# Kernel tuning notes

Hardware: AMD Instinct MI355X
Metric: run time of the kernel (lower is better)

## Reference

```python
import jax, jax.numpy as jnp
import numpy as np

B, N, DE, DH, L, DC = 8, 256, 768, 192, 2, 192
NEG = 1e30  # mask_logic constant from the repo


def setup_inputs() -> dict:
    ks = iter(jax.random.split(jax.random.key(0), 32))

    def nrm(shape, s=0.02):
        return jax.random.normal(next(ks), shape, dtype=jnp.float32) * s

    features = jax.random.normal(next(ks), (B, N, DE), dtype=jnp.float32)
    # DAG adjacency: node i attends to a subset of j < i; guarantee edge (i, i-1)
    rnd = jax.random.bernoulli(next(ks), 0.3, (B, N, N))
    tril = jnp.tril(jnp.ones((N, N), jnp.bool_), -1)
    adj = ((rnd & tril[None]) | jnp.eye(N, k=-1, dtype=jnp.bool_)[None]).astype(jnp.float32)
    s_mask = jax.random.bernoulli(next(ks), 0.5, (B, N, N)).astype(jnp.float32)
    s_mask_onehot = jnp.stack([1.0 - s_mask, s_mask], axis=-1)  # unused in forward
    lengths = jnp.full((B,), N, dtype=jnp.int32)  # unused (nodal_att_type=None)
    return dict(
        features=features, adj=adj, s_mask=s_mask,
        s_mask_onehot=s_mask_onehot, lengths=lengths,
        fc1_w=nrm((DE, DH)), fc1_b=jnp.zeros((DH,), jnp.float32),
        gat_w=nrm((L, 2 * DH)), gat_b=jnp.zeros((L,), jnp.float32),
        wr0=nrm((L, DH, DH)), wr1=nrm((L, DH, DH)),
        gruc_wih=nrm((L, 3 * DH, DH)), gruc_whh=nrm((L, 3 * DH, DH)),
        gruc_bih=jnp.zeros((L, 3 * DH), jnp.float32),
        gruc_bhh=jnp.zeros((L, 3 * DH), jnp.float32),
        grup_wih=nrm((L, 3 * DH, DH)), grup_whh=nrm((L, 3 * DH, DH)),
        grup_bih=jnp.zeros((L, 3 * DH), jnp.float32),
        grup_bhh=jnp.zeros((L, 3 * DH), jnp.float32),
        mlp_w0=nrm((DH * (L + 1), DH)), mlp_b0=jnp.zeros((DH,), jnp.float32),
        mlp_w1=nrm((DH, DH)), mlp_b1=jnp.zeros((DH,), jnp.float32),
        mlp_w2=nrm((DH, DC)), mlp_b2=jnp.zeros((DC,), jnp.float32),
    )


def _gru(x, h, wih, whh, bih, bhh):
    # torch.nn.GRUCell math
    gi = x @ wih.T + bih
    gh = h @ whh.T + bhh
    ir, iz, inn = jnp.split(gi, 3, axis=-1)
    hr, hz, hn = jnp.split(gh, 3, axis=-1)
    r = jax.nn.sigmoid(ir + hr)
    z = jax.nn.sigmoid(iz + hz)
    n = jnp.tanh(inn + r * hn)
    return (1.0 - z) * n + z * h


def _layer(Hl, adj, s_mask, gat_w, gat_b, wr0, wr1, cw, cp):
    # One DAG layer: sequential scan over nodes. Carry holds the relation-
    # projected value buffers V0=H1@Wr0^T, V1=H1@Wr1^T and per-node key
    # scores Ksc=H1@wk (rows >= i are zero and masked out), which is
    # mathematically identical to the torch code that re-projects the
    # growing H1 every step.
    wq, wk = gat_w[:DH], gat_w[DH:]
    pos = jnp.arange(N)

    def step(carry, xs):
        V0, V1, Ksc = carry
        i, x_i, adj_i, sm_i = xs  # x_i:(B,DH) adj_i,sm_i:(B,N)
        score = (x_i @ wq)[:, None] + Ksc + gat_b          # (B,N)
        mask = (pos < i)[None, :] & (adj_i > 0.5)          # ragged :i slice
        alpha = jnp.where(mask, score, score - NEG)        # mask_logic
        attn = jax.nn.softmax(alpha, axis=-1)              # masked -> exactly 0
        Vrel = V0 * sm_i[..., None] + V1 * (1.0 - sm_i[..., None])
        M = jnp.einsum('bn,bnd->bd', attn, Vrel)
        M = jnp.where(i > 0, M, 0.0)                       # node 0: no context
        C = _gru(x_i, M, *cw)
        P = _gru(M, x_i, *cp)
        Hnew = C + P
        V0 = V0.at[:, i, :].set(Hnew @ wr0.T)
        V1 = V1.at[:, i, :].set(Hnew @ wr1.T)
        Ksc = Ksc.at[:, i].set(Hnew @ wk)
        attn_out = jnp.where(i > 0, attn, 0.0)             # adjB row 0 is zeros
        return (V0, V1, Ksc), (Hnew, attn_out)

    z3 = jnp.zeros((B, N, DH), jnp.float32)
    carry0 = (z3, z3, jnp.zeros((B, N), jnp.float32))
    xs = (pos, Hl.transpose(1, 0, 2), adj.transpose(1, 0, 2), s_mask.transpose(1, 0, 2))
    _, (Hseq, Aseq) = jax.lax.scan(step, carry0, xs)
    return Hseq.transpose(1, 0, 2), Aseq.transpose(1, 0, 2)  # (B,N,DH),(B,N,N)


def reference(features, adj, s_mask, s_mask_onehot, lengths,
              fc1_w, fc1_b, gat_w, gat_b, wr0, wr1,
              gruc_wih, gruc_whh, gruc_bih, gruc_bhh,
              grup_wih, grup_whh, grup_bih, grup_bhh,
              mlp_w0, mlp_b0, mlp_w1, mlp_b1, mlp_w2, mlp_b2):
    Hl = jax.nn.relu(features @ fc1_w + fc1_b)  # H0
    Hs, As = [Hl], []
    for l in range(L):
        cw = (gruc_wih[l], gruc_whh[l], gruc_bih[l], gruc_bhh[l])
        cp = (grup_wih[l], grup_whh[l], grup_bih[l], grup_bhh[l])
        Hl, Al = _layer(Hl, adj, s_mask, gat_w[l], gat_b[l], wr0[l], wr1[l], cw, cp)
        Hs.append(Hl)
        As.append(Al)
    H = jnp.concatenate(Hs, axis=2)  # (B,N,DH*(L+1))
    # nodal_att_type=None => attentive_node_features is identity
    h = jax.nn.relu(H @ mlp_w0 + mlp_b0)
    h = jax.nn.relu(h @ mlp_w1 + mlp_b1)  # mlp_layers-1 = 1 extra block
    logits = h @ mlp_w2 + mlp_b2          # dropout: eval-mode identity
    return logits, jnp.stack(As, axis=1)  # (B,N,DC), (B,L,N,N)
```

## Files before the change

kernel.cpp:

```cpp
#include <hip/hip_runtime.h>
#include <stdint.h>

#define B_  8
#define N_  256
#define DH_ 192
#define L_  2
#define G3  576
#define G6  1152
#define NW  4
#define DS  48
#define KD  24
#define GC  288
#define STH 10001
#define STP 20001
#define STQ 25001
#define SPK 50000
#define SF1 50001
#define SF2 50002
#define SDN 60001

typedef unsigned long long u64;

__device__ __forceinline__ float bflo(uint32_t u) { return __uint_as_float(u << 16); }
__device__ __forceinline__ float bfhi(uint32_t u) { return __uint_as_float(u & 0xffff0000u); }
__device__ __forceinline__ uint32_t f2bf(float f) {
    uint32_t x = __float_as_uint(f);
    x += 0x7fffu + ((x >> 16) & 1u);
    return x >> 16;
}
__device__ __forceinline__ float sigm(float x)  { return 1.f / (1.f + __expf(-x)); }
__device__ __forceinline__ float tanhf_(float x){ return 1.f - 2.f / (1.f + __expf(2.f * x)); }
__device__ __forceinline__ u64 packvs(float v, int st) {
    return ((u64)(uint32_t)st << 32) | __float_as_uint(v);
}
__device__ __forceinline__ u64 agload(const u64* p) {
    return __hip_atomic_load(p, __ATOMIC_RELAXED, __HIP_MEMORY_SCOPE_AGENT);
}
__device__ __forceinline__ void agstore(u64* p, u64 v) {
    __hip_atomic_store(p, v, __ATOMIC_RELAXED, __HIP_MEMORY_SCOPE_AGENT);
}

struct ScanSm {
    uint4 Wlds4[24 * GC];
    uint4 Wr4s[12 * DH_];
    float sA0[N_], sA1[N_], sKsc[N_];
    float sAdjN[N_], sSmN[N_];
    float sXq[DH_], sPre[6 * DS], sXv[DS];
    float sM[DH_], su0[DS], su1[DS], sGc[GC], sHn[DS];
    float sRedS[4], sRedX[3], sSaved[4];
};
struct WorkSm {
    uint4 Wp4[24 * GC];
    float sX[DH_];
    float sPv[GC];
    float sRed[3];
};
struct PrologSm {
    float sA[8][768];
    float sRed[3][8][192];
};
struct MlpSm {
    float sH[8][576];
    float sRed[3][8][192];
    float sT[8][192];
};

__device__ void prepack_slice(int idx,
    const float* __restrict__ wr0, const float* __restrict__ wr1,
    const float* __restrict__ c_wih, const float* __restrict__ c_whh,
    const float* __restrict__ c_bih, const float* __restrict__ c_bhh,
    const float* __restrict__ p_wih, const float* __restrict__ p_whh,
    const float* __restrict__ p_bih, const float* __restrict__ p_bhh,
    float* __restrict__ WpreT, uint32_t* __restrict__ W4,
    uint32_t* __restrict__ Wr4, uint32_t* __restrict__ Wp4w,
    float* __restrict__ biasPre, float* __restrict__ gbx)
{
    for (int l = 0; l < L_; ++l) {
        const float* cwih = c_wih + l * G3 * DH_;
        const float* cwhh = c_whh + l * G3 * DH_;
        const float* pwih = p_wih + l * G3 * DH_;
        const float* pwhh = p_whh + l * G3 * DH_;
        if (l == 0) {
            int k = idx / G6, r = idx - k * G6;
            float w = (r < G3) ? cwih[r * DH_ + k] : pwhh[(r - G3) * DH_ + k];
            WpreT[k * G6 + r] = w;
        }
        if (idx < NW * 27648) {
            int w = idx / 27648, pos = idx % 27648;
            int p4 = pos / 1152, rem = pos % 1152;
            int c2 = rem >> 2, s = rem & 3;
            int p = 4 * p4 + s;
            int j = c2 / DS, dd = c2 % DS;
            int c = 192 * j + DS * w + dd;
            float w0 = (c < G3) ? cwhh[c * DH_ + 2 * p]     : pwih[(c - G3) * DH_ + 2 * p];
            float w1 = (c < G3) ? cwhh[c * DH_ + 2 * p + 1] : pwih[(c - G3) * DH_ + 2 * p + 1];
            W4[l * NW * 27648 + idx] = f2bf(w0) | (f2bf(w1) << 16);
            if (l == 1) {
                int r = c;
                float v0 = (r < G3) ? cwih[r * DH_ + 2 * p]     : pwhh[(r - G3) * DH_ + 2 * p];
                float v1 = (r < G3) ? cwih[r * DH_ + 2 * p + 1] : pwhh[(r - G3) * DH_ + 2 * p + 1];
                Wp4w[idx] = f2bf(v0) | (f2bf(v1) << 16);
            }
        }
        if (idx < NW * 9216) {
            int w = idx / 9216, pos = idx % 9216;
            int kq = pos / 768, rem = pos % 768;
            int d = rem >> 2, s = rem & 3;
            int k = DS * w + 4 * kq + s;
            Wr4[l * NW * 9216 + idx] =
                f2bf(wr0[l * DH_ * DH_ + d * DH_ + k]) |
                (f2bf(wr1[l * DH_ * DH_ + d * DH_ + k]) << 16);
        }
        if (idx < G6) {
            float base = (idx < G3) ? c_bih[l * G3 + idx] : p_bhh[l * G3 + idx - G3];
            float fold = 0.f;
            if (idx < 384)                    fold = c_bhh[l * G3 + idx];
            else if (idx >= G3 && idx < 960)  fold = p_bih[l * G3 + idx - G3];
            biasPre[l * G6 + idx] = base + fold;
        }
        if (idx < 384) {
            gbx[l * 384 + idx] = (idx < DH_) ? c_bhh[l * G3 + 384 + idx]
                                             : p_bih[l * G3 + 384 + (idx - DH_)];
        }
    }
}

__device__ void flag_sync(u64* flags, int wgid, int t, int stamp)
{
    __threadfence();
    __syncthreads();
    if (t == 0) agstore(&flags[wgid], packvs(0.f, stamp));
    if (t < 96) {
        while ((uint32_t)(agload(&flags[t]) >> 32) != (uint32_t)stamp) {}
    }
    __syncthreads();
    __threadfence();
    __syncthreads();
}

__device__ void prologue(char* smem, int wgid, int t,
    const float* __restrict__ features, const float* __restrict__ fc1_w,
    const float* __restrict__ fc1_b, const float* __restrict__ WpreT,
    const float* __restrict__ biasPre,
    float* __restrict__ Hcat, float* __restrict__ PREg, u64* __restrict__ Fp)
{
    PrologSm* P = (PrologSm*)smem;
    const int c = t % 192, kg = t / 192;
    for (int tt = wgid; tt < 256; tt += 96) {
        const int r0 = tt * 8;
        for (int q = t; q < 1536; q += 576) {
            int r = q / 192, c4 = q % 192;
            *(float4*)&P->sA[r][4 * c4] = *(const float4*)(features + (size_t)(r0 + r) * 768 + 4 * c4);
        }
        __syncthreads();
        {
            const float* bp = fc1_w + (size_t)(kg * 256) * 192 + c;
            float acc[8] = {0.f, 0.f, 0.f, 0.f, 0.f, 0.f, 0.f, 0.f};
            #pragma unroll 8
            for (int kk = 0; kk < 256; ++kk) {
                float bv = bp[(size_t)kk * 192];
                #pragma unroll
                for (int rr = 0; rr < 8; ++rr) acc[rr] += P->sA[rr][kg * 256 + kk] * bv;
            }
            #pragma unroll
            for (int rr = 0; rr < 8; ++rr) P->sRed[kg][rr][c] = acc[rr];
        }
        __syncthreads();
        if (t < 192) {
            float bv = fc1_b[t];
            #pragma unroll
            for (int rr = 0; rr < 8; ++rr) {
                float v = P->sRed[0][rr][t] + P->sRed[1][rr][t] + P->sRed[2][rr][t] + bv;
                Hcat[(size_t)(r0 + rr) * G3 + t] = fmaxf(v, 0.f);
            }
        }
        __syncthreads();
    }
    flag_sync(Fp + 96, wgid, t, SF1);
    {
        const float bpa = biasPre[t], bpb = biasPre[576 + t];
        for (int tt = wgid; tt < 256; tt += 96) {
            const int r0 = tt * 8;
            for (int q = t; q < 384; q += 576) {
                int r = q / 48, c4 = q % 48;
                *(float4*)&P->sA[r][4 * c4] = *(const float4*)(Hcat + (size_t)(r0 + r) * G3 + 4 * c4);
            }
            __syncthreads();
            {
                const float* b0 = WpreT + t;
                float a0[8] = {0.f,0.f,0.f,0.f,0.f,0.f,0.f,0.f};
                float a1[8] = {0.f,0.f,0.f,0.f,0.f,0.f,0.f,0.f};
                #pragma unroll 4
                for (int k = 0; k < 192; ++k) {
                    float bva = b0[(size_t)k * G6];
                    float bvb = b0[(size_t)k * G6 + 576];
                    #pragma unroll
                    for (int rr = 0; rr < 8; ++rr) {
                        float av = P->sA[rr][k];
                        a0[rr] += av * bva; a1[rr] += av * bvb;
                    }
                }
                #pragma unroll
                for (int rr = 0; rr < 8; ++rr) {
                    PREg[(size_t)(r0 + rr) * G6 + t]       = a0[rr] + bpa;
                    PREg[(size_t)(r0 + rr) * G6 + 576 + t] = a1[rr] + bpb;
                }
            }
            __syncthreads();
        }
    }
    flag_sync(Fp + 192, wgid, t, SF2);
}

__device__ void mlp_tail(char* smem, int wgid, int t,
    const float* __restrict__ Hcat,
    const float* __restrict__ mw0, const float* __restrict__ mb0,
    const float* __restrict__ mw1, const float* __restrict__ mb1,
    const float* __restrict__ mw2, const float* __restrict__ mb2,
    float* __restrict__ out, u64* __restrict__ Fd)
{
    if (t < 64) {
        while ((uint32_t)(agload(&Fd[t]) >> 32) != (uint32_t)SDN) {}
    }
    __syncthreads();
    __threadfence();
    __syncthreads();
    MlpSm* M = (MlpSm*)smem;
    const int c = t % 192, kg = t / 192;
    for (int tt = wgid; tt < 256; tt += 96) {
        const int r0 = tt * 8;
        for (int q = t; q < 1152; q += 576) {
            int r = q / 144, c4 = q % 144;
            *(float4*)&M->sH[r][4 * c4] = *(const float4*)(Hcat + (size_t)(r0 + r) * G3 + 4 * c4);
        }
        __syncthreads();
        {
            const float* bp = mw0 + (size_t)(kg * 192) * 192 + c;
            float acc[8] = {0.f,0.f,0.f,0.f,0.f,0.f,0.f,0.f};
            #pragma unroll 8
            for (int kk = 0; kk < 192; ++kk) {
                float bv = bp[(size_t)kk * 192];
                #pragma unroll
                for (int rr = 0; rr < 8; ++rr) acc[rr] += M->sH[rr][kg * 192 + kk] * bv;
            }
            #pragma unroll
            for (int rr = 0; rr < 8; ++rr) M->sRed[kg][rr][c] = acc[rr];
        }
        __syncthreads();
        if (t < 192) {
            float bv = mb0[t];
            #pragma unroll
            for (int rr = 0; rr < 8; ++rr)
                M->sT[rr][t] = fmaxf(M->sRed[0][rr][t] + M->sRed[1][rr][t] + M->sRed[2][rr][t] + bv, 0.f);
        }
        __syncthreads();
        {
            const float* bp = mw1 + (size_t)(kg * 64) * 192 + c;
            float acc[8] = {0.f,0.f,0.f,0.f,0.f,0.f,0.f,0.f};
            #pragma unroll 8
            for (int kk = 0; kk < 64; ++kk) {
                float bv = bp[(size_t)kk * 192];
                #pragma unroll
                for (int rr = 0; rr < 8; ++rr) acc[rr] += M->sT[rr][kg * 64 + kk] * bv;
            }
            #pragma unroll
            for (int rr = 0; rr < 8; ++rr) M->sRed[kg][rr][c] = acc[rr];
        }
        __syncthreads();
        if (t < 192) {
            float bv = mb1[t];
            #pragma unroll
            for (int rr = 0; rr < 8; ++rr)
                M->sH[rr][t] = fmaxf(M->sRed[0][rr][t] + M->sRed[1][rr][t] + M->sRed[2][rr][t] + bv, 0.f);
        }
        __syncthreads();
        {
            const float* bp = mw2 + (size_t)(kg * 64) * 192 + c;
            float acc[8] = {0.f,0.f,0.f,0.f,0.f,0.f,0.f,0.f};
            #pragma unroll 8
            for (int kk = 0; kk < 64; ++kk) {
                float bv = bp[(size_t)kk * 192];
                #pragma unroll
                for (int rr = 0; rr < 8; ++rr) acc[rr] += M->sH[rr][kg * 64 + kk] * bv;
            }
            #pragma unroll
            for (int rr = 0; rr < 8; ++rr) M->sRed[kg][rr][c] = acc[rr];
        }
        __syncthreads();
        if (t < 192) {
            float bv = mb2[t];
            #pragma unroll
            for (int rr = 0; rr < 8; ++rr)
                out[(size_t)(r0 + rr) * 192 + t] =
                    M->sRed[0][rr][t] + M->sRed[1][rr][t] + M->sRed[2][rr][t] + bv;
        }
        __syncthreads();
    }
}

template<int ISL2>
__device__ void scan_body(
    ScanSm* S, int b, int w, int t,
    const float* __restrict__ xin, float* __restrict__ hout,
    const float* __restrict__ PREg, const float* __restrict__ adj,
    const float* __restrict__ smask,
    const uint32_t* __restrict__ W4l, const uint32_t* __restrict__ Wr4l,
    const float* __restrict__ gbxl, const float* __restrict__ gatwl,
    uint32_t* __restrict__ Hw, u64* __restrict__ MPsl, u64* __restrict__ Kdl,
    u64* __restrict__ HcW, const u64* __restrict__ HcR,
    const u64* __restrict__ PREcR, const u64* __restrict__ XQcR,
    float* __restrict__ AsB, int sbase)
{
    const int lane = t & 63, wave = t >> 6;
    const int dg0 = w * DS;
    const float* adjB = adj   + (size_t)b * N_ * N_;
    const float* smB  = smask + (size_t)b * N_ * N_;
    const int fi = b * NW;

    {
        uint32_t* wl = (uint32_t*)S->Wlds4;
        for (int q = t; q < 27648; q += 576) wl[q] = W4l[q];
        uint32_t* wr = (uint32_t*)S->Wr4s;
        for (int q = t; q < 9216; q += 576) wr[q] = Wr4l[q];
    }
    float wqv = (!ISL2 && t < DH_) ? gatwl[t] : 0.f;
    float wkv = 0.f, g2b = 0.f, g5b = 0.f;
    if (t < DS) { wkv = gatwl[DH_ + dg0 + t]; g2b = gbxl[dg0 + t]; g5b = gbxl[DH_ + dg0 + t]; }
    if (t < N_) S->sKsc[t] = 0.f;
    if (w == 0 && t < N_) AsB[t] = 0.f;

    if (!ISL2) {
        if (t < DS) {
            const float* pre = PREg + (size_t)(b * N_) * G6 + dg0 + t;
            S->sPre[t] = pre[0]; S->sPre[DS + t] = pre[192]; S->sPre[2 * DS + t] = pre[384];
            S->sPre[3 * DS + t] = pre[576]; S->sPre[4 * DS + t] = pre[768]; S->sPre[5 * DS + t] = pre[960];
            S->sXv[t] = xin[(size_t)(b * N_) * G3 + dg0 + t];
        }
        for (int q = t; q < 176; q += 576) {
            if (q < 64)       *(float4*)&S->sAdjN[4 * q] = *(const float4*)(adjB + N_ + 4 * q);
            else if (q < 128) { int q2 = q - 64;  *(float4*)&S->sSmN[4 * q2] = *(const float4*)(smB + N_ + 4 * q2); }
            else              { int q2 = q - 128; *(float4*)&S->sXq[4 * q2] = *(const float4*)(xin + (size_t)(b * N_ + 1) * G3 + 4 * q2); }
        }
    } else {
        for (int q = t; q < 321; q += 576) {
            if (q < 64)       *(float4*)&S->sAdjN[4 * q] = *(const float4*)(adjB + N_ + 4 * q);
            else if (q < 128) { int q2 = q - 64;  *(float4*)&S->sSmN[4 * q2] = *(const float4*)(smB + N_ + 4 * q2); }
            else if (q < 176) {
                int d = q - 128;
                const u64* p = HcR + ((size_t)(b * N_) * NW + w) * DS + d;
                u64 v; do { v = agload(p); } while ((uint32_t)(v >> 32) != (uint32_t)STH);
                S->sXv[d] = __uint_as_float((uint32_t)v);
            } else if (q < 320) {
                int qq = q - 176;
                const u64* p = PREcR + ((size_t)(b * N_) * NW + w) * 144 + qq;
                u64 v; do { v = agload(p); } while ((uint32_t)(v >> 32) != (uint32_t)STP);
                uint32_t pl = (uint32_t)v;
                S->sPre[2 * qq] = bflo(pl); S->sPre[2 * qq + 1] = bfhi(pl);
            } else {
                const u64* p = XQcR + b * N_ + 1;
                u64 v; do { v = agload(p); } while ((uint32_t)(v >> 32) != (uint32_t)(STQ + 1));
                S->sSaved[3] = __uint_as_float((uint32_t)v);
            }
        }
    }
    __syncthreads();
    {
        float hn = 0.f;
        if (t < DS) {
            float xv = S->sXv[t];
            float r1 = sigm(S->sPre[t]), z1 = sigm(S->sPre[DS + t]);
            float n1 = tanhf_(S->sPre[2 * DS + t] + r1 * g2b);
            float Cv = (1.f - z1) * n1;
            float r2 = sigm(S->sPre[3 * DS + t]), z2 = sigm(S->sPre[4 * DS + t]);
            float n2 = tanhf_(g5b + r2 * S->sPre[5 * DS + t]);
            hn = Cv + (1.f - z2) * n2 + z2 * xv;
            S->sHn[t] = hn;
            hout[(size_t)(b * N_) * G3 + dg0 + t] = hn;
            if (!ISL2) HcW[((size_t)(b * N_) * NW + w) * DS + t] = packvs(hn, STH);
        }
        if (wave == 0) {
            float v = hn * wkv;
            #pragma unroll
            for (int o = 32; o; o >>= 1) v += __shfl_xor(v, o);
            if (lane == 0) agstore(&Kdl[fi + w], packvs(v, sbase));
        }
    }
    __syncthreads();
    if (t < KD) Hw[(size_t)t * N_] = f2bf(S->sHn[2 * t]) | (f2bf(S->sHn[2 * t + 1]) << 16);
    if (!ISL2) {
        float px = (t < DH_) ? S->sXq[t] * wqv : 0.f;
        #pragma unroll
        for (int o = 32; o; o >>= 1) px += __shfl_xor(px, o);
        if (t < DH_ && lane == 0) S->sRedX[wave] = px;
    }
    __syncthreads();
    float xq = ISL2 ? S->sSaved[3] : (S->sRedX[0] + S->sRedX[1] + S->sRedX[2]);

    for (int i = 1; i < N_; ++i) {
        const int row = b * N_ + i;
        const int stamp = sbase + i;
        {
            float e = 0.f;
            if (t == i - 1) { S->sSaved[0] = S->sAdjN[t]; S->sSaved[1] = S->sSmN[t]; }
            if (t < N_) {
                if (t < i - 1 && S->sAdjN[t] > 0.5f) e = __expf(xq + S->sKsc[t]);
                float b0 = e * S->sSmN[t];
                S->sA0[t] = b0; S->sA1[t] = e - b0;
            }
            float ps = e;
            #pragma unroll
            for (int o = 32; o; o >>= 1) ps += __shfl_xor(ps, o);
            if (t < N_ && lane == 0) S->sRedS[wave] = ps;
        }
        __syncthreads();
        if (t < 384) {
            const int ilim = i - 1;
            const int kd = t >> 4, jp = t & 15;
            const uint32_t* hp = Hw + (size_t)kd * N_;
            float u0l = 0.f, u0h = 0.f, u1l = 0.f, u1h = 0.f;
            int j = jp;
            while (j + 48 < ilim) {
                uint32_t h0 = hp[j], h1 = hp[j + 16], h2 = hp[j + 32], h3 = hp[j + 48];
                float b0, b1;
                b0 = S->sA0[j];      b1 = S->sA1[j];
                u0l = fmaf(b0, bflo(h0), u0l); u0h = fmaf(b0, bfhi(h0), u0h);
                u1l = fmaf(b1, bflo(h0), u1l); u1h = fmaf(b1, bfhi(h0), u1h);
                b0 = S->sA0[j + 16]; b1 = S->sA1[j + 16];
                u0l = fmaf(b0, bflo(h1), u0l); u0h = fmaf(b0, bfhi(h1), u0h);
                u1l = fmaf(b1, bflo(h1), u1l); u1h = fmaf(b1, bfhi(h1), u1h);
                b0 = S->sA0[j + 32]; b1 = S->sA1[j + 32];
                u0l = fmaf(b0, bflo(h2), u0l); u0h = fmaf(b0, bfhi(h2), u0h);
                u1l = fmaf(b1, bflo(h2), u1l); u1h = fmaf(b1, bfhi(h2), u1h);
                b0 = S->sA0[j + 48]; b1 = S->sA1[j + 48];
                u0l = fmaf(b0, bflo(h3), u0l); u0h = fmaf(b0, bfhi(h3), u0h);
                u1l = fmaf(b1, bflo(h3), u1l); u1h = fmaf(b1, bfhi(h3), u1h);
                j += 64;
            }
            for (; j < ilim; j += 16) {
                uint32_t hv = hp[j];
                float b0 = S->sA0[j], b1 = S->sA1[j];
                u0l = fmaf(b0, bflo(hv), u0l); u0h = fmaf(b0, bfhi(hv), u0h);
                u1l = fmaf(b1, bflo(hv), u1l); u1h = fmaf(b1, bfhi(hv), u1h);
            }
            #pragma unroll
            for (int o = 1; o <= 8; o <<= 1) {
                u0l += __shfl_xor(u0l, o); u0h += __shfl_xor(u0h, o);
                u1l += __shfl_xor(u1l, o); u1h += __shfl_xor(u1h, o);
            }
            if (jp == 0) {
                S->su0[2 * kd] = u0l; S->su0[2 * kd + 1] = u0h;
                S->su1[2 * kd] = u1l; S->su1[2 * kd + 1] = u1h;
            }
        } else {
            const int u = t - 384;
            const int inx = (i + 1 < N_) ? i + 1 : N_ - 1;
            if (!ISL2) {
                for (int q = u; q < 260; q += 192) {
                    if (q < 64)
                        *(float4*)&S->sAdjN[4 * q] = *(const float4*)(adjB + (size_t)inx * N_ + 4 * q);
                    else if (q < 128) { int q2 = q - 64;
                        *(float4*)&S->sSmN[4 * q2] = *(const float4*)(smB + (size_t)inx * N_ + 4 * q2); }
                    else if (q < 140) { int q2 = q - 128;
                        *(float4*)&S->sXv[4 * q2] = *(const float4*)(xin + (size_t)row * G3 + dg0 + 4 * q2); }
                    else if (q < 212) { int q2 = q - 140; int g = q2 / 12, o = q2 - 12 * g;
                        *(float4*)&S->sPre[g * DS + 4 * o] =
                            *(const float4*)(PREg + (size_t)row * G6 + g * DH_ + dg0 + 4 * o); }
                    else { int q2 = q - 212;
                        *(float4*)&S->sXq[4 * q2] = *(const float4*)(xin + (size_t)(b * N_ + inx) * G3 + 4 * q2); }
                }
            } else {
                for (int q = u; q < 321; q += 192) {
                    if (q < 64)
                        *(float4*)&S->sAdjN[4 * q] = *(const float4*)(adjB + (size_t)inx * N_ + 4 * q);
                    else if (q < 128) { int q2 = q - 64;
                        *(float4*)&S->sSmN[4 * q2] = *(const float4*)(smB + (size_t)inx * N_ + 4 * q2); }
                    else if (q < 176) {
                        int d = q - 128;
                        const u64* p = HcR + ((size_t)row * NW + w) * DS + d;
                        u64 v; do { v = agload(p); } while ((uint32_t)(v >> 32) != (uint32_t)(STH + i));
                        S->sXv[d] = __uint_as_float((uint32_t)v);
                    } else if (q < 320) {
                        int qq = q - 176;
                        const u64* p = PREcR + ((size_t)row * NW + w) * 144 + qq;
                        u64 v; do { v = agload(p); } while ((uint32_t)(v >> 32) != (uint32_t)(STP + i));
                        uint32_t pl = (uint32_t)v;
                        S->sPre[2 * qq] = bflo(pl); S->sPre[2 * qq + 1] = bfhi(pl);
                    } else {
                        const u64* p = XQcR + b * N_ + inx;
                        u64 v; do { v = agload(p); } while ((uint32_t)(v >> 32) != (uint32_t)(STQ + inx));
                        S->sSaved[3] = __uint_as_float((uint32_t)v);
                    }
                }
            }
            if (t == 575) {
                const uint32_t ex = (uint32_t)(stamp - 1);
                u64 k0, k1, k2, k3;
                do {
                    k0 = agload(&Kdl[fi + 0]); k1 = agload(&Kdl[fi + 1]);
                    k2 = agload(&Kdl[fi + 2]); k3 = agload(&Kdl[fi + 3]);
                } while ((uint32_t)(k0 >> 32) != ex || (uint32_t)(k1 >> 32) != ex ||
                         (uint32_t)(k2 >> 32) != ex || (uint32_t)(k3 >> 32) != ex);
                float kdot = __uint_as_float((uint32_t)k0) + __uint_as_float((uint32_t)k1)
                           + __uint_as_float((uint32_t)k2) + __uint_as_float((uint32_t)k3);
                float adjI1 = S->sSaved[0], smI1 = S->sSaved[1];
                float e1 = (adjI1 > 0.5f) ? __expf(xq + kdot) : 0.f;
                float Ssum = S->sRedS[0] + S->sRedS[1] + S->sRedS[2] + S->sRedS[3] + e1;
                S->sKsc[i - 1] = kdot;
                float c0 = e1 * smI1;
                S->sA0[i - 1] = c0; S->sA1[i - 1] = e1 - c0;
                S->sSaved[2] = 1.f / Ssum;
            }
        }
        __syncthreads();
        if (t < DH_) {
            float mp = 0.f, h0a = 0.f, h1a = 0.f;
            #pragma unroll 4
            for (int kq = 0; kq < 12; ++kq) {
                uint4 wv = S->Wr4s[kq * DH_ + t];
                const int k0 = 4 * kq;
                float lo, hi;
                lo = bflo(wv.x); hi = bfhi(wv.x);
                mp = fmaf(S->su0[k0 + 0], lo, mp); mp = fmaf(S->su1[k0 + 0], hi, mp);
                h0a = fmaf(S->sHn[k0 + 0], lo, h0a); h1a = fmaf(S->sHn[k0 + 0], hi, h1a);
                lo = bflo(wv.y); hi = bfhi(wv.y);
                mp = fmaf(S->su0[k0 + 1], lo, mp); mp = fmaf(S->su1[k0 + 1], hi, mp);
                h0a = fmaf(S->sHn[k0 + 1], lo, h0a); h1a = fmaf(S->sHn[k0 + 1], hi, h1a);
                lo = bflo(wv.z); hi = bfhi(wv.z);
                mp = fmaf(S->su0[k0 + 2], lo, mp); mp = fmaf(S->su1[k0 + 2], hi, mp);
                h0a = fmaf(S->sHn[k0 + 2], lo, h0a); h1a = fmaf(S->sHn[k0 + 2], hi, h1a);
                lo = bflo(wv.w); hi = bfhi(wv.w);
                mp = fmaf(S->su0[k0 + 3], lo, mp); mp = fmaf(S->su1[k0 + 3], hi, mp);
                h0a = fmaf(S->sHn[k0 + 3], lo, h0a); h1a = fmaf(S->sHn[k0 + 3], hi, h1a);
            }
            float invS = S->sSaved[2];
            mp = (mp + S->sA0[i - 1] * h0a + S->sA1[i - 1] * h1a) * invS;
            agstore(&MPsl[(size_t)(fi + w) * DH_ + t], packvs(mp, stamp));
            const int w1 = (w + 1) & 3, w2 = (w + 2) & 3, w3 = (w + 3) & 3;
            u64* pA = &MPsl[(size_t)(fi + w1) * DH_ + t];
            u64* pB = &MPsl[(size_t)(fi + w2) * DH_ + t];
            u64* pC = &MPsl[(size_t)(fi + w3) * DH_ + t];
            const uint32_t ex = (uint32_t)stamp;
            u64 vA, vB, vC;
            do {
                vA = agload(pA); vB = agload(pB); vC = agload(pC);
            } while ((uint32_t)(vA >> 32) != ex || (uint32_t)(vB >> 32) != ex ||
                     (uint32_t)(vC >> 32) != ex);
            S->sM[t] = mp + __uint_as_float((uint32_t)vA)
                          + __uint_as_float((uint32_t)vB)
                          + __uint_as_float((uint32_t)vC);
        } else if (w == 0 && t < 448) {
            int j = t - 192;
            AsB[(size_t)i * N_ + j] = (S->sA0[j] + S->sA1[j]) * S->sSaved[2];
        }
        __syncthreads();
        {
            const int c = t >> 1, kh = t & 1;
            const uint4* wp = S->Wlds4 + (12 * kh) * GC + c;
            float g = 0.f;
            #pragma unroll 4
            for (int p4 = 0; p4 < 12; ++p4) {
                uint4 wv = wp[p4 * GC];
                const int m0 = 8 * (12 * kh + p4);
                g = fmaf(S->sM[m0 + 0], bflo(wv.x), g); g = fmaf(S->sM[m0 + 1], bfhi(wv.x), g);
                g = fmaf(S->sM[m0 + 2], bflo(wv.y), g); g = fmaf(S->sM[m0 + 3], bfhi(wv.y), g);
                g = fmaf(S->sM[m0 + 4], bflo(wv.z), g); g = fmaf(S->sM[m0 + 5], bfhi(wv.z), g);
                g = fmaf(S->sM[m0 + 6], bflo(wv.w), g); g = fmaf(S->sM[m0 + 7], bfhi(wv.w), g);
            }
            g += __shfl_xor(g, 1);
            if (kh == 0) S->sGc[c] = g;
        }
        __syncthreads();
        {
            float hn = 0.f;
            if (t < DS) {
                float Mv = S->sM[dg0 + t];
                float r1 = sigm(S->sPre[t] + S->sGc[t]);
                float z1 = sigm(S->sPre[DS + t] + S->sGc[DS + t]);
                float n1 = tanhf_(S->sPre[2 * DS + t] + r1 * (S->sGc[2 * DS + t] + g2b));
                float Cv = (1.f - z1) * n1 + z1 * Mv;
                float r2 = sigm(S->sGc[3 * DS + t] + S->sPre[3 * DS + t]);
                float z2 = sigm(S->sGc[4 * DS + t] + S->sPre[4 * DS + t]);
                float n2 = tanhf_(S->sGc[5 * DS + t] + g5b + r2 * S->sPre[5 * DS + t]);
                hn = Cv + (1.f - z2) * n2 + z2 * S->sXv[t];
                S->sHn[t] = hn;
                hout[(size_t)row * G3 + dg0 + t] = hn;
                if (!ISL2) HcW[((size_t)row * NW + w) * DS + t] = packvs(hn, STH + i);
            }
            if (wave == 0) {
                float v = hn * wkv;
                #pragma unroll
                for (int o = 32; o; o >>= 1) v += __shfl_xor(v, o);
                if (lane == 0) agstore(&Kdl[fi + w], packvs(v, stamp));
            }
            if (t < KD) Hw[(size_t)t * N_ + i] = f2bf(S->sHn[2 * t]) | (f2bf(S->sHn[2 * t + 1]) << 16);
            if (!ISL2) {
                float px = (t < DH_) ? S->sXq[t] * wqv : 0.f;
                #pragma unroll
                for (int o = 32; o; o >>= 1) px += __shfl_xor(px, o);
                if (t < DH_ && lane == 0) S->sRedX[wave] = px;
            }
        }
        __syncthreads();
        xq = ISL2 ? S->sSaved[3] : (S->sRedX[0] + S->sRedX[1] + S->sRedX[2]);
    }
}

__device__ void worker_body(WorkSm* Wm, int b, int w, int t,
    const uint32_t* __restrict__ Wp4g, const float* __restrict__ bias2,
    const float* __restrict__ wq2,
    const u64* __restrict__ HcR, u64* __restrict__ PREcW, u64* __restrict__ XQcW)
{
    const int lane = t & 63, wave = t >> 6;
    { uint32_t* wl = (uint32_t*)Wm->Wp4; for (int q = t; q < 27648; q += 576) wl[q] = Wp4g[q]; }
    const int c = t >> 1, kh = t & 1;
    float bv = 0.f;
    if (kh == 0) bv = bias2[192 * (c / DS) + w * DS + (c % DS)];
    float wqt = (t < DH_) ? wq2[t] : 0.f;
    for (int i = 0; i < N_; ++i) {
        if (t < DH_) {
            const u64* p = HcR + ((size_t)(b * N_ + i) * NW + (t / DS)) * DS + (t % DS);
            u64 v; do { v = agload(p); } while ((uint32_t)(v >> 32) != (uint32_t)(STH + i));
            Wm->sX[t] = __uint_as_float((uint32_t)v);
        }
        __syncthreads();
        {
            const uint4* wp = Wm->Wp4 + (12 * kh) * GC + c;
            float g = 0.f;
            #pragma unroll 4
            for (int p4 = 0; p4 < 12; ++p4) {
                uint4 wv = wp[p4 * GC];
                const int m0 = 8 * (12 * kh + p4);
                g = fmaf(Wm->sX[m0 + 0], bflo(wv.x), g); g = fmaf(Wm->sX[m0 + 1], bfhi(wv.x), g);
                g = fmaf(Wm->sX[m0 + 2], bflo(wv.y), g); g = fmaf(Wm->sX[m0 + 3], bfhi(wv.y), g);
                g = fmaf(Wm->sX[m0 + 4], bflo(wv.z), g); g = fmaf(Wm->sX[m0 + 5], bfhi(wv.z), g);
                g = fmaf(Wm->sX[m0 + 6], bflo(wv.w), g); g = fmaf(Wm->sX[m0 + 7], bfhi(wv.w), g);
            }
            g += __shfl_xor(g, 1);
            if (kh == 0) Wm->sPv[c] = g + bv;
        }
        if (w == 0) {
            float px = (t < DH_) ? Wm->sX[t] * wqt : 0.f;
            #pragma unroll
            for (int o = 32; o; o >>= 1) px += __shfl_xor(px, o);
            if (t < DH_ && lane == 0) Wm->sRed[wave] = px;
        }
        __syncthreads();
        if (t < 144) {
            u64 v = ((u64)(uint32_t)(STP + i) << 32)
                  | f2bf(Wm->sPv[2 * t]) | (f2bf(Wm->sPv[2 * t + 1]) << 16);
            agstore(&PREcW[((size_t)(b * N_ + i) * NW + w) * 144 + t], v);
        }
        if (w == 0 && t == 0)
            agstore(&XQcW[b * N_ + i],
                    packvs(Wm->sRed[0] + Wm->sRed[1] + Wm->sRed[2], STQ + i));
        __syncthreads();
    }
}

__global__ __launch_bounds__(576, 1) void pipeline_kernel(
    const float* __restrict__ features, const float* __restrict__ fc1_w,
    const float* __restrict__ fc1_b,
    const float* __restrict__ adj, const float* __restrict__ smask,
    const float* __restrict__ gatw,
    const float* __restrict__ wr0, const float* __restrict__ wr1,
    const float* __restrict__ c_wih, const float* __restrict__ c_whh,
    const float* __restrict__ c_bih, const float* __restrict__ c_bhh,
    const float* __restrict__ p_wih, const float* __restrict__ p_whh,
    const float* __restrict__ p_bih, const float* __restrict__ p_bhh,
    const float* __restrict__ mw0, const float* __restrict__ mb0,
    const float* __restrict__ mw1, const float* __restrict__ mb1,
    const float* __restrict__ mw2, const float* __restrict__ mb2,
    float* __restrict__ Hcat, float* __restrict__ PREg,
    float* __restrict__ WpreT, uint32_t* __restrict__ W4,
    uint32_t* __restrict__ Wr4, uint32_t* __restrict__ Wp4w,
    float* __restrict__ biasPre, float* __restrict__ gbx,
    uint32_t* __restrict__ Hb, u64* __restrict__ MPs, u64* __restrict__ Kd,
    u64* __restrict__ Hc, u64* __restrict__ PREc, u64* __restrict__ XQc,
    u64* __restrict__ Fp, u64* __restrict__ Fd,
    float* __restrict__ out)
{
    __shared__ __align__(16) char smem[sizeof(ScanSm)];
    const int blk = blockIdx.x, t = threadIdx.x;
    const int wgid = blk;
    const int b = blk & 7, r12 = blk >> 3;
    const int role = r12 >> 2, w = r12 & 3;

    for (int j = 0; j < 4; ++j) {
        int idx = wgid * 576 + t + 55296 * j;
        prepack_slice(idx, wr0, wr1, c_wih, c_whh, c_bih, c_bhh,
                      p_wih, p_whh, p_bih, p_bhh,
                      WpreT, W4, Wr4, Wp4w, biasPre, gbx);
    }
    flag_sync(Fp, wgid, t, SPK);

    prologue(smem, wgid, t, features, fc1_w, fc1_b, WpreT, biasPre,
             Hcat, PREg, Fp);

    float* As = out + 393216;
    if (role == 0) {
        scan_body<0>((ScanSm*)smem, b, w, t,
            Hcat, Hcat + 192, PREg, adj, smask,
            W4, Wr4, gbx, gatw,
            Hb + (size_t)(b * NW + w) * KD * N_, MPs, Kd,
            Hc, nullptr, nullptr, nullptr,
            As + (size_t)b * (L_ * N_ * N_), 1);
        __threadfence();
        __syncthreads();
        if (t == 0) agstore(&Fd[b * 8 + w], packvs(0.f, SDN));
    } else if (role == 2) {
        scan_body<1>((ScanSm*)smem, b, w, t,
            nullptr, Hcat + 384, nullptr, adj, smask,
            W4 + NW * 27648, Wr4 + NW * 9216, gbx + 384, gatw + 384,
            Hb + (size_t)(32 + b * NW + w) * KD * N_,
            MPs + (size_t)8 * NW * DH_, Kd + 8 * NW,
            nullptr, Hc, PREc, XQc,
            As + (size_t)b * (L_ * N_ * N_) + N_ * N_, 30001);
        __threadfence();
        __syncthreads();
        if (t == 0) agstore(&Fd[b * 8 + 4 + w], packvs(0.f, SDN));
    } else {
        worker_body((WorkSm*)smem, b, w, t,
            Wp4w + (size_t)w * 27648, biasPre + G6, gatw + 384,
            Hc, PREc, XQc);
    }

    mlp_tail(smem, wgid, t, Hcat, mw0, mb0, mw1, mb1, mw2, mb2, out, Fd);
}

extern "C" void kernel_launch(void* const* d_in, const int* in_sizes, int n_in,
                              void* d_out, int out_size, void* d_ws, size_t ws_size,
                              hipStream_t stream)
{
    const float* features = (const float*)d_in[0];
    const float* adj      = (const float*)d_in[1];
    const float* smask    = (const float*)d_in[2];
    const float* fc1_w = (const float*)d_in[5];
    const float* fc1_b = (const float*)d_in[6];
    const float* gat_w = (const float*)d_in[7];
    const float* wr0   = (const float*)d_in[9];
    const float* wr1   = (const float*)d_in[10];
    const float* c_wih = (const float*)d_in[11];
    const float* c_whh = (const float*)d_in[12];
    const float* c_bih = (const float*)d_in[13];
    const float* c_bhh = (const float*)d_in[14];
    const float* p_wih = (const float*)d_in[15];
    const float* p_whh = (const float*)d_in[16];
    const float* p_bih = (const float*)d_in[17];
    const float* p_bhh = (const float*)d_in[18];
    const float* mw0 = (const float*)d_in[19];
    const float* mb0 = (const float*)d_in[20];
    const float* mw1 = (const float*)d_in[21];
    const float* mb1 = (const float*)d_in[22];
    const float* mw2 = (const float*)d_in[23];
    const float* mb2 = (const float*)d_in[24];
    float* out = (float*)d_out;

    char* wsb = (char*)d_ws;
    size_t off = 0;
    auto carve = [&](size_t bytes) -> char* {
        char* p = wsb + off;
        off = (off + bytes + 255) & ~(size_t)255;
        return p;
    };
    float* Hcat     = (float*)carve(2048ull * 576 * 4);
    float* PREg     = (float*)carve(2048ull * 1152 * 4);
    float* WpreT    = (float*)carve(192ull * 1152 * 4);
    uint32_t* W4    = (uint32_t*)carve(2ull * NW * 27648 * 4);
    uint32_t* Wr4   = (uint32_t*)carve(2ull * NW * 9216 * 4);
    uint32_t* Wp4w  = (uint32_t*)carve((size_t)NW * 27648 * 4);
    float* biasPre  = (float*)carve(2ull * 1152 * 4);
    float* gbx      = (float*)carve(2ull * 384 * 4);
    uint32_t* Hb    = (uint32_t*)carve(64ull * KD * 256 * 4);
    u64* MPs        = (u64*)carve(2ull * 8 * NW * DH_ * 8);
    u64* Kd         = (u64*)carve(2ull * 8 * NW * 8);
    u64* Hc         = (u64*)carve(8ull * 256 * NW * DS * 8);
    u64* PREc       = (u64*)carve(8ull * 256 * NW * 144 * 8);
    u64* XQc        = (u64*)carve(8ull * 256 * 8);
    u64* Fp         = (u64*)carve(288ull * 8);
    u64* Fd         = (u64*)carve(64ull * 8);

    pipeline_kernel<<<dim3(96), 576, 0, stream>>>(
        features, fc1_w, fc1_b, adj, smask, gat_w,
        wr0, wr1, c_wih, c_whh, c_bih, c_bhh, p_wih, p_whh, p_bih, p_bhh,
        mw0, mb0, mw1, mb1, mw2, mb2,
        Hcat, PREg, WpreT, W4, Wr4, Wp4w, biasPre, gbx,
        Hb, MPs, Kd, Hc, PREc, XQc, Fp, Fd, out);
}
```

Baseline: 1.915 ms.

## Keep GRU weights in registers and reorder scan steps to overlap cross-block wait

The bf16 GRU weight slices used in the per-node matvec now stay in registers (12 uint4 per thread) instead of being staged in LDS, in both the scan and worker roles. This cuts LDS traffic and shrinks shared memory. The scan loop is also reordered with double-buffered attention arrays: the next node's softmax numerators and the weighted H reduction are computed while waves 6-8 poll other blocks' partial message sums. This hides the cross-block spin latency, at the cost of higher register pressure and a more intricate sync order.

```diff
diff --git a/kernel.cpp b/kernel.cpp
--- a/kernel.cpp
+++ b/kernel.cpp
@@ -41,16 +41,14 @@
 }
 
 struct ScanSm {
-    uint4 Wlds4[24 * GC];
     uint4 Wr4s[12 * DH_];
-    float sA0[N_], sA1[N_], sKsc[N_];
+    float sA0[2][N_], sA1[2][N_], sKsc[N_];
     float sAdjN[N_], sSmN[N_];
     float sXq[DH_], sPre[6 * DS], sXv[DS];
     float sM[DH_], su0[DS], su1[DS], sGc[GC], sHn[DS];
-    float sRedS[4], sRedX[3], sSaved[4];
+    float sRedS[2][4], sRedX[3], sSaved[4];
 };
 struct WorkSm {
-    uint4 Wp4[24 * GC];
     float sX[DH_];
     float sPv[GC];
     float sRed[3];
@@ -64,6 +62,7 @@
     float sRed[3][8][192];
     float sT[8][192];
 };
+union SmemAll { ScanSm s; WorkSm w; PrologSm p; MlpSm m; };
 
 __device__ void prepack_slice(int idx,
     const float* __restrict__ wr0, const float* __restrict__ wr1,
@@ -316,17 +315,24 @@
     const float* adjB = adj   + (size_t)b * N_ * N_;
     const float* smB  = smask + (size_t)b * N_ * N_;
     const int fi = b * NW;
+    const int cB4 = t >> 1, khB4 = t & 1;
 
     {
-        uint32_t* wl = (uint32_t*)S->Wlds4;
-        for (int q = t; q < 27648; q += 576) wl[q] = W4l[q];
         uint32_t* wr = (uint32_t*)S->Wr4s;
         for (int q = t; q < 9216; q += 576) wr[q] = Wr4l[q];
+    }
+    uint4 wreg[12];
+    {
+        const uint4* W4v = (const uint4*)W4l;
+        #pragma unroll
+        for (int p4 = 0; p4 < 12; ++p4) wreg[p4] = W4v[(12 * khB4 + p4) * GC + cB4];
     }
     float wqv = (!ISL2 && t < DH_) ? gatwl[t] : 0.f;
     float wkv = 0.f, g2b = 0.f, g5b = 0.f;
     if (t < DS) { wkv = gatwl[DH_ + dg0 + t]; g2b = gbxl[dg0 + t]; g5b = gbxl[DH_ + dg0 + t]; }
-    if (t < N_) S->sKsc[t] = 0.f;
+    if (t < N_) { S->sKsc[t] = 0.f; S->sA0[1][t] = 0.f; S->sA1[1][t] = 0.f; }
+    if (t < DS) { S->su0[t] = 0.f; S->su1[t] = 0.f; }
+    if (t < 4)  S->sRedS[1][t] = 0.f;
     if (w == 0 && t < N_) AsB[t] = 0.f;
 
     if (!ISL2) {
@@ -378,6 +384,7 @@
             hout[(size_t)(b * N_) * G3 + dg0 + t] = hn;
             if (!ISL2) HcW[((size_t)(b * N_) * NW + w) * DS + t] = packvs(hn, STH);
         }
+        if (t == 0) { S->sSaved[0] = S->sAdjN[0]; S->sSaved[1] = S->sSmN[0]; }
         if (wave == 0) {
             float v = hn * wkv;
             #pragma unroll
@@ -394,97 +401,47 @@
         if (t < DH_ && lane == 0) S->sRedX[wave] = px;
     }
     __syncthreads();
-    float xq = ISL2 ? S->sSaved[3] : (S->sRedX[0] + S->sRedX[1] + S->sRedX[2]);
+    float xqc = ISL2 ? S->sSaved[3] : (S->sRedX[0] + S->sRedX[1] + S->sRedX[2]);
 
     for (int i = 1; i < N_; ++i) {
         const int row = b * N_ + i;
         const int stamp = sbase + i;
-        {
-            float e = 0.f;
-            if (t == i - 1) { S->sSaved[0] = S->sAdjN[t]; S->sSaved[1] = S->sSmN[t]; }
-            if (t < N_) {
-                if (t < i - 1 && S->sAdjN[t] > 0.5f) e = __expf(xq + S->sKsc[t]);
-                float b0 = e * S->sSmN[t];
-                S->sA0[t] = b0; S->sA1[t] = e - b0;
-            }
-            float ps = e;
-            #pragma unroll
-            for (int o = 32; o; o >>= 1) ps += __shfl_xor(ps, o);
-            if (t < N_ && lane == 0) S->sRedS[wave] = ps;
-        }
-        __syncthreads();
-        if (t < 384) {
-            const int ilim = i - 1;
-            const int kd = t >> 4, jp = t & 15;
-            const uint32_t* hp = Hw + (size_t)kd * N_;
-            float u0l = 0.f, u0h = 0.f, u1l = 0.f, u1h = 0.f;
-            int j = jp;
-            while (j + 48 < ilim) {
-                uint32_t h0 = hp[j], h1 = hp[j + 16], h2 = hp[j + 32], h3 = hp[j + 48];
-                float b0, b1;
-                b0 = S->sA0[j];      b1 = S->sA1[j];
-                u0l = fmaf(b0, bflo(h0), u0l); u0h = fmaf(b0, bfhi(h0), u0h);
-                u1l = fmaf(b1, bflo(h0), u1l); u1h = fmaf(b1, bfhi(h0), u1h);
-                b0 = S->sA0[j + 16]; b1 = S->sA1[j + 16];
-                u0l = fmaf(b0, bflo(h1), u0l); u0h = fmaf(b0, bfhi(h1), u0h);
-                u1l = fmaf(b1, bflo(h1), u1l); u1h = fmaf(b1, bfhi(h1), u1h);
-                b0 = S->sA0[j + 32]; b1 = S->sA1[j + 32];
-                u0l = fmaf(b0, bflo(h2), u0l); u0h = fmaf(b0, bfhi(h2), u0h);
-                u1l = fmaf(b1, bflo(h2), u1l); u1h = fmaf(b1, bfhi(h2), u1h);
-                b0 = S->sA0[j + 48]; b1 = S->sA1[j + 48];
-                u0l = fmaf(b0, bflo(h3), u0l); u0h = fmaf(b0, bfhi(h3), u0h);
-                u1l = fmaf(b1, bflo(h3), u1l); u1h = fmaf(b1, bfhi(h3), u1h);
-                j += 64;
-            }
-            for (; j < ilim; j += 16) {
-                uint32_t hv = hp[j];
-                float b0 = S->sA0[j], b1 = S->sA1[j];
-                u0l = fmaf(b0, bflo(hv), u0l); u0h = fmaf(b0, bfhi(hv), u0h);
-                u1l = fmaf(b1, bflo(hv), u1l); u1h = fmaf(b1, bfhi(hv), u1h);
-            }
-            #pragma unroll
-            for (int o = 1; o <= 8; o <<= 1) {
-                u0l += __shfl_xor(u0l, o); u0h += __shfl_xor(u0h, o);
-                u1l += __shfl_xor(u1l, o); u1h += __shfl_xor(u1h, o);
-            }
-            if (jp == 0) {
-                S->su0[2 * kd] = u0l; S->su0[2 * kd + 1] = u0h;
-                S->su1[2 * kd] = u1l; S->su1[2 * kd + 1] = u1h;
-            }
-        } else {
+        const int pp = i & 1, pn = pp ^ 1;
+
+        if (t >= 384) {
             const int u = t - 384;
             const int inx = (i + 1 < N_) ? i + 1 : N_ - 1;
             if (!ISL2) {
-                for (int q = u; q < 260; q += 192) {
-                    if (q < 64)
-                        *(float4*)&S->sAdjN[4 * q] = *(const float4*)(adjB + (size_t)inx * N_ + 4 * q);
-                    else if (q < 128) { int q2 = q - 64;
+                for (int qq = u; qq < 260; qq += 192) {
+                    if (qq < 64)
+                        *(float4*)&S->sAdjN[4 * qq] = *(const float4*)(adjB + (size_t)inx * N_ + 4 * qq);
+                    else if (qq < 128) { int q2 = qq - 64;
                         *(float4*)&S->sSmN[4 * q2] = *(const float4*)(smB + (size_t)inx * N_ + 4 * q2); }
-                    else if (q < 140) { int q2 = q - 128;
+                    else if (qq < 140) { int q2 = qq - 128;
                         *(float4*)&S->sXv[4 * q2] = *(const float4*)(xin + (size_t)row * G3 + dg0 + 4 * q2); }
-                    else if (q < 212) { int q2 = q - 140; int g = q2 / 12, o = q2 - 12 * g;
+                    else if (qq < 212) { int q2 = qq - 140; int g = q2 / 12, o = q2 - 12 * g;
                         *(float4*)&S->sPre[g * DS + 4 * o] =
                             *(const float4*)(PREg + (size_t)row * G6 + g * DH_ + dg0 + 4 * o); }
-                    else { int q2 = q - 212;
+                    else { int q2 = qq - 212;
                         *(float4*)&S->sXq[4 * q2] = *(const float4*)(xin + (size_t)(b * N_ + inx) * G3 + 4 * q2); }
                 }
             } else {
-                for (int q = u; q < 321; q += 192) {
-                    if (q < 64)
-                        *(float4*)&S->sAdjN[4 * q] = *(const float4*)(adjB + (size_t)inx * N_ + 4 * q);
-                    else if (q < 128) { int q2 = q - 64;
+                for (int qq = u; qq < 321; qq += 192) {
+                    if (qq < 64)
+                        *(float4*)&S->sAdjN[4 * qq] = *(const float4*)(adjB + (size_t)inx * N_ + 4 * qq);
+                    else if (qq < 128) { int q2 = qq - 64;
                         *(float4*)&S->sSmN[4 * q2] = *(const float4*)(smB + (size_t)inx * N_ + 4 * q2); }
-                    else if (q < 176) {
-                        int d = q - 128;
+                    else if (qq < 176) {
+                        int d = qq - 128;
                         const u64* p = HcR + ((size_t)row * NW + w) * DS + d;
                         u64 v; do { v = agload(p); } while ((uint32_t)(v >> 32) != (uint32_t)(STH + i));
                         S->sXv[d] = __uint_as_float((uint32_t)v);
-                    } else if (q < 320) {
-                        int qq = q - 176;
-                        const u64* p = PREcR + ((size_t)row * NW + w) * 144 + qq;
+                    } else if (qq < 320) {
+                        int q2 = qq - 176;
+                        const u64* p = PREcR + ((size_t)row * NW + w) * 144 + q2;
                         u64 v; do { v = agload(p); } while ((uint32_t)(v >> 32) != (uint32_t)(STP + i));
                         uint32_t pl = (uint32_t)v;
-                        S->sPre[2 * qq] = bflo(pl); S->sPre[2 * qq + 1] = bfhi(pl);
+                        S->sPre[2 * q2] = bflo(pl); S->sPre[2 * q2 + 1] = bfhi(pl);
                     } else {
                         const u64* p = XQcR + b * N_ + inx;
                         u64 v; do { v = agload(p); } while ((uint32_t)(v >> 32) != (uint32_t)(STQ + inx));
@@ -503,15 +460,16 @@
                 float kdot = __uint_as_float((uint32_t)k0) + __uint_as_float((uint32_t)k1)
                            + __uint_as_float((uint32_t)k2) + __uint_as_float((uint32_t)k3);
                 float adjI1 = S->sSaved[0], smI1 = S->sSaved[1];
-                float e1 = (adjI1 > 0.5f) ? __expf(xq + kdot) : 0.f;
-                float Ssum = S->sRedS[0] + S->sRedS[1] + S->sRedS[2] + S->sRedS[3] + e1;
+                float e1 = (adjI1 > 0.5f) ? __expf(xqc + kdot) : 0.f;
+                float Ssum = S->sRedS[pp][0] + S->sRedS[pp][1] + S->sRedS[pp][2] + S->sRedS[pp][3] + e1;
                 S->sKsc[i - 1] = kdot;
                 float c0 = e1 * smI1;
-                S->sA0[i - 1] = c0; S->sA1[i - 1] = e1 - c0;
+                S->sA0[pp][i - 1] = c0; S->sA1[pp][i - 1] = e1 - c0;
                 S->sSaved[2] = 1.f / Ssum;
             }
         }
         __syncthreads();
+
         if (t < DH_) {
             float mp = 0.f, h0a = 0.f, h1a = 0.f;
             #pragma unroll 4
@@ -533,43 +491,107 @@
                 h0a = fmaf(S->sHn[k0 + 3], lo, h0a); h1a = fmaf(S->sHn[k0 + 3], hi, h1a);
             }
             float invS = S->sSaved[2];
-            mp = (mp + S->sA0[i - 1] * h0a + S->sA1[i - 1] * h1a) * invS;
+            mp = (mp + S->sA0[pp][i - 1] * h0a + S->sA1[pp][i - 1] * h1a) * invS;
+            S->sM[t] = mp;
             agstore(&MPsl[(size_t)(fi + w) * DH_ + t], packvs(mp, stamp));
+            if (!ISL2) {
+                float px = S->sXq[t] * wqv;
+                #pragma unroll
+                for (int o = 32; o; o >>= 1) px += __shfl_xor(px, o);
+                if (lane == 0) S->sRedX[wave] = px;
+            }
+        } else if (w == 0 && t < 448) {
+            int j = t - 192;
+            AsB[(size_t)i * N_ + j] = (S->sA0[pp][j] + S->sA1[pp][j]) * S->sSaved[2];
+        }
+        __syncthreads();
+
+        const float xqn = ISL2 ? S->sSaved[3] : (S->sRedX[0] + S->sRedX[1] + S->sRedX[2]);
+        if (t < N_) {
+            float e = 0.f;
+            if (t == i) { S->sSaved[0] = S->sAdjN[t]; S->sSaved[1] = S->sSmN[t]; }
+            if (t < i && S->sAdjN[t] > 0.5f) e = __expf(xqn + S->sKsc[t]);
+            float b0 = e * S->sSmN[t];
+            S->sA0[pn][t] = b0; S->sA1[pn][t] = e - b0;
+            float ps = e;
+            #pragma unroll
+            for (int o = 32; o; o >>= 1) ps += __shfl_xor(ps, o);
+            if (lane == 0) S->sRedS[pn][wave] = ps;
+        }
+        __syncthreads();
+
+        if (t < 384) {
+            const int ilim = i;
+            const int kd = t >> 4, jp = t & 15;
+            const uint32_t* hp = Hw + (size_t)kd * N_;
+            float u0l = 0.f, u0h = 0.f, u1l = 0.f, u1h = 0.f;
+            int j = jp;
+            while (j + 48 < ilim) {
+                uint32_t h0 = hp[j], h1 = hp[j + 16], h2 = hp[j + 32], h3 = hp[j + 48];
+                float b0, b1;
+                b0 = S->sA0[pn][j];      b1 = S->sA1[pn][j];
+                u0l = fmaf(b0, bflo(h0), u0l); u0h = fmaf(b0, bfhi(h0), u0h);
+                u1l = fmaf(b1, bflo(h0), u1l); u1h = fmaf(b1, bfhi(h0), u1h);
+                b0 = S->sA0[pn][j + 16]; b1 = S->sA1[pn][j + 16];
+                u0l = fmaf(b0, bflo(h1), u0l); u0h = fmaf(b0, bfhi(h1), u0h);
+                u1l = fmaf(b1, bflo(h1), u1l); u1h = fmaf(b1, bfhi(h1), u1h);
+                b0 = S->sA0[pn][j + 32]; b1 = S->sA1[pn][j + 32];
+                u0l = fmaf(b0, bflo(h2), u0l); u0h = fmaf(b0, bfhi(h2), u0h);
+                u1l = fmaf(b1, bflo(h2), u1l); u1h = fmaf(b1, bfhi(h2), u1h);
+                b0 = S->sA0[pn][j + 48]; b1 = S->sA1[pn][j + 48];
+                u0l = fmaf(b0, bflo(h3), u0l); u0h = fmaf(b0, bfhi(h3), u0h);
+                u1l = fmaf(b1, bflo(h3), u1l); u1h = fmaf(b1, bfhi(h3), u1h);
+                j += 64;
+            }
+            for (; j < ilim; j += 16) {
+                uint32_t hv = hp[j];
+                float b0 = S->sA0[pn][j], b1 = S->sA1[pn][j];
+                u0l = fmaf(b0, bflo(hv), u0l); u0h = fmaf(b0, bfhi(hv), u0h);
+                u1l = fmaf(b1, bflo(hv), u1l); u1h = fmaf(b1, bfhi(hv), u1h);
+            }
+            #pragma unroll
+            for (int o = 1; o <= 8; o <<= 1) {
+                u0l += __shfl_xor(u0l, o); u0h += __shfl_xor(u0h, o);
+                u1l += __shfl_xor(u1l, o); u1h += __shfl_xor(u1h, o);
+            }
+            if (jp == 0) {
+                S->su0[2 * kd] = u0l; S->su0[2 * kd + 1] = u0h;
+                S->su1[2 * kd] = u1l; S->su1[2 * kd + 1] = u1h;
+            }
+        } else {
+            const int d = t - 384;
             const int w1 = (w + 1) & 3, w2 = (w + 2) & 3, w3 = (w + 3) & 3;
-            u64* pA = &MPsl[(size_t)(fi + w1) * DH_ + t];
-            u64* pB = &MPsl[(size_t)(fi + w2) * DH_ + t];
-            u64* pC = &MPsl[(size_t)(fi + w3) * DH_ + t];
+            u64* pA = &MPsl[(size_t)(fi + w1) * DH_ + d];
+            u64* pB = &MPsl[(size_t)(fi + w2) * DH_ + d];
+            u64* pC = &MPsl[(size_t)(fi + w3) * DH_ + d];
             const uint32_t ex = (uint32_t)stamp;
             u64 vA, vB, vC;
             do {
                 vA = agload(pA); vB = agload(pB); vC = agload(pC);
             } while ((uint32_t)(vA >> 32) != ex || (uint32_t)(vB >> 32) != ex ||
                      (uint32_t)(vC >> 32) != ex);
-            S->sM[t] = mp + __uint_as_float((uint32_t)vA)
-                          + __uint_as_float((uint32_t)vB)
-                          + __uint_as_float((uint32_t)vC);
-        } else if (w == 0 && t < 448) {
-            int j = t - 192;
-            AsB[(size_t)i * N_ + j] = (S->sA0[j] + S->sA1[j]) * S->sSaved[2];
-        }
-        __syncthreads();
+            S->sM[d] += __uint_as_float((uint32_t)vA)
+                      + __uint_as_float((uint32_t)vB)
+                      + __uint_as_float((uint32_t)vC);
+        }
+        __syncthreads();
+
         {
-            const int c = t >> 1, kh = t & 1;
-            const uint4* wp = S->Wlds4 + (12 * kh) * GC + c;
             float g = 0.f;
-            #pragma unroll 4
+            #pragma unroll
             for (int p4 = 0; p4 < 12; ++p4) {
-                uint4 wv = wp[p4 * GC];
-                const int m0 = 8 * (12 * kh + p4);
+                const uint4 wv = wreg[p4];
+                const int m0 = 8 * (12 * khB4 + p4);
                 g = fmaf(S->sM[m0 + 0], bflo(wv.x), g); g = fmaf(S->sM[m0 + 1], bfhi(wv.x), g);
                 g = fmaf(S->sM[m0 + 2], bflo(wv.y), g); g = fmaf(S->sM[m0 + 3], bfhi(wv.y), g);
                 g = fmaf(S->sM[m0 + 4], bflo(wv.z), g); g = fmaf(S->sM[m0 + 5], bfhi(wv.z), g);
                 g = fmaf(S->sM[m0 + 6], bflo(wv.w), g); g = fmaf(S->sM[m0 + 7], bfhi(wv.w), g);
             }
             g += __shfl_xor(g, 1);
-            if (kh == 0) S->sGc[c] = g;
-        }
-        __syncthreads();
+            if (khB4 == 0) S->sGc[cB4] = g;
+        }
+        __syncthreads();
+
         {
             float hn = 0.f;
             if (t < DS) {
@@ -593,15 +615,9 @@
                 if (lane == 0) agstore(&Kdl[fi + w], packvs(v, stamp));
             }
             if (t < KD) Hw[(size_t)t * N_ + i] = f2bf(S->sHn[2 * t]) | (f2bf(S->sHn[2 * t + 1]) << 16);
-            if (!ISL2) {
-                float px = (t < DH_) ? S->sXq[t] * wqv : 0.f;
-                #pragma unroll
-                for (int o = 32; o; o >>= 1) px += __shfl_xor(px, o);
-                if (t < DH_ && lane == 0) S->sRedX[wave] = px;
-            }
-        }
-        __syncthreads();
-        xq = ISL2 ? S->sSaved[3] : (S->sRedX[0] + S->sRedX[1] + S->sRedX[2]);
+        }
+        __syncthreads();
+        xqc = xqn;
     }
 }
 
@@ -611,8 +627,13 @@
     const u64* __restrict__ HcR, u64* __restrict__ PREcW, u64* __restrict__ XQcW)
 {
     const int lane = t & 63, wave = t >> 6;
-    { uint32_t* wl = (uint32_t*)Wm->Wp4; for (int q = t; q < 27648; q += 576) wl[q] = Wp4g[q]; }
     const int c = t >> 1, kh = t & 1;
+    uint4 wpreg[12];
+    {
+        const uint4* v4 = (const uint4*)Wp4g;
+        #pragma unroll
+        for (int p4 = 0; p4 < 12; ++p4) wpreg[p4] = v4[(12 * kh + p4) * GC + c];
+    }
     float bv = 0.f;
     if (kh == 0) bv = bias2[192 * (c / DS) + w * DS + (c % DS)];
     float wqt = (t < DH_) ? wq2[t] : 0.f;
@@ -624,11 +645,10 @@
         }
         __syncthreads();
         {
-            const uint4* wp = Wm->Wp4 + (12 * kh) * GC + c;
             float g = 0.f;
-            #pragma unroll 4
+            #pragma unroll
             for (int p4 = 0; p4 < 12; ++p4) {
-                uint4 wv = wp[p4 * GC];
+                const uint4 wv = wpreg[p4];
                 const int m0 = 8 * (12 * kh + p4);
                 g = fmaf(Wm->sX[m0 + 0], bflo(wv.x), g); g = fmaf(Wm->sX[m0 + 1], bfhi(wv.x), g);
                 g = fmaf(Wm->sX[m0 + 2], bflo(wv.y), g); g = fmaf(Wm->sX[m0 + 3], bfhi(wv.y), g);
@@ -679,7 +699,7 @@
     u64* __restrict__ Fp, u64* __restrict__ Fd,
     float* __restrict__ out)
 {
-    __shared__ __align__(16) char smem[sizeof(ScanSm)];
+    __shared__ __align__(16) char smem[sizeof(SmemAll)];
     const int blk = blockIdx.x, t = threadIdx.x;
     const int wgid = blk;
     const int b = blk & 7, r12 = blk >> 3;
```

Result: no change. 1.932 ms (+0.9%).
